# Optimization experiments

Hardware: AMD Instinct MI355X
Metric: run time of the kernel (lower is better)

## Reference

```python
import jax, jax.numpy as jnp
import numpy as np

NUM_EMBEDDINGS = 4096
EMBEDDING_DIM = 256


def setup_inputs() -> dict:
    key = jax.random.key(0)
    k1, k2 = jax.random.split(key)
    inputs = jax.random.normal(k1, (16, 4096, EMBEDDING_DIM), dtype=jnp.float32)
    embeddings = jax.random.normal(k2, (NUM_EMBEDDINGS, EMBEDDING_DIM), dtype=jnp.float32)
    return {"inputs": inputs, "embeddings": embeddings}


def reference(inputs, embeddings):
    input_shape = inputs.shape
    flat = inputs.reshape(-1, EMBEDDING_DIM)                     # [N, D]
    input_sq = jnp.sum(flat * flat, axis=1, keepdims=True)       # [N, 1]
    emb_sq = jnp.sum(embeddings * embeddings, axis=1)            # [K]
    distances = input_sq - 2.0 * (flat @ embeddings.T) + emb_sq  # [N, K]
    encoding_indices = jnp.argmin(distances, axis=1)             # [N]
    quantized = embeddings[encoding_indices].reshape(input_shape)
    encoding_indices = encoding_indices.reshape(input_shape[:-1])
    # use_commitment=False path: codebook loss only (quantized detached)
    loss = jnp.mean((jax.lax.stop_gradient(quantized) - inputs) ** 2)
    # straight-through estimator
    quantized_st = inputs + jax.lax.stop_gradient(quantized - inputs)
    return (quantized_st, loss, encoding_indices)
```

## Files before the change

### kernel.cpp

```cpp
#include <hip/hip_runtime.h>
#include <float.h>
#include <stdint.h>


#define DDIM 256
#define KCODES 4096
#define NROWS 65536
#define QSIZE 16777216
#define NSLOT 64
#define NLBLK 16384
#define GAP_THRESH 0.02f

#define O_FCOUNT 4097
#define O_FLAGS 4100
#define O_IDXF 69636
#define O_LPART 135172
#define O_EMBH 151556
#define O_EMBL 675844
#define O_AH 1200384
#define O_AL 9588992
#define O_KEYS 17977600
#define WS_NEED_FLOATS 18108672ull

typedef short bf16x8 __attribute__((ext_vector_type(8)));
typedef float f32x4 __attribute__((ext_vector_type(4)));

__device__ __forceinline__ void gload_lds16(const void* g, void* l) {
    __builtin_amdgcn_global_load_lds(
        (const __attribute__((address_space(1))) void*)g,
        (__attribute__((address_space(3))) void*)l, 16, 0, 0);
}

__global__ __launch_bounds__(64) void esq_conv(const float* __restrict__ emb,
                                               float* __restrict__ ws,
                                               short* __restrict__ eh,
                                               short* __restrict__ el) {
    int c = blockIdx.x, l = threadIdx.x;
    const float4* e4 = (const float4*)(emb + (size_t)c * DDIM);
    float4 v = e4[l];
    float s = v.x * v.x + v.y * v.y + v.z * v.z + v.w * v.w;
    float f[4] = {v.x, v.y, v.z, v.w};
    uint32_t hu[4], lu[4];
#pragma unroll
    for (int k = 0; k < 4; ++k) {
        uint32_t u = __float_as_uint(f[k]);
        uint32_t h = u & 0xFFFF0000u;
        hu[k] = h;
        lu[k] = __float_as_uint(f[k] - __uint_as_float(h));
    }
    uint2 hv, lv;
    hv.x = __builtin_amdgcn_perm(hu[1], hu[0], 0x07060302u);
    hv.y = __builtin_amdgcn_perm(hu[3], hu[2], 0x07060302u);
    lv.x = __builtin_amdgcn_perm(lu[1], lu[0], 0x07060302u);
    lv.y = __builtin_amdgcn_perm(lu[3], lu[2], 0x07060302u);
    *(uint2*)&eh[(size_t)c * DDIM + l * 4] = hv;
    *(uint2*)&el[(size_t)c * DDIM + l * 4] = lv;
#pragma unroll
    for (int off = 32; off >= 1; off >>= 1) s += __shfl_down(s, off);
    if (l == 0) ws[c] = s;
    if (c == 0 && l == 0) ((int*)ws)[O_FCOUNT] = 0;
}

__device__ __forceinline__ void conv8(float4 a, float4 b,
                                      short* __restrict__ dh,
                                      short* __restrict__ dl) {
    float f[8] = {a.x, a.y, a.z, a.w, b.x, b.y, b.z, b.w};
    uint32_t hu[8], lu[8];
#pragma unroll
    for (int k = 0; k < 8; ++k) {
        uint32_t u = __float_as_uint(f[k]);
        uint32_t h = u & 0xFFFF0000u;
        hu[k] = h;
        lu[k] = __float_as_uint(f[k] - __uint_as_float(h));
    }
    uint4 hv, lv;
    hv.x = __builtin_amdgcn_perm(hu[1], hu[0], 0x07060302u);
    hv.y = __builtin_amdgcn_perm(hu[3], hu[2], 0x07060302u);
    hv.z = __builtin_amdgcn_perm(hu[5], hu[4], 0x07060302u);
    hv.w = __builtin_amdgcn_perm(hu[7], hu[6], 0x07060302u);
    lv.x = __builtin_amdgcn_perm(lu[1], lu[0], 0x07060302u);
    lv.y = __builtin_amdgcn_perm(lu[3], lu[2], 0x07060302u);
    lv.z = __builtin_amdgcn_perm(lu[5], lu[4], 0x07060302u);
    lv.w = __builtin_amdgcn_perm(lu[7], lu[6], 0x07060302u);
    *(uint4*)dh = hv;
    *(uint4*)dl = lv;
}

__device__ __forceinline__ void stage8(const float* __restrict__ p,
                                       short* __restrict__ dh,
                                       short* __restrict__ dl) {
    float4 a = *(const float4*)p;
    float4 b = *(const float4*)(p + 4);
    conv8(a, b, dh, dl);
}

__global__ __launch_bounds__(256) void inp_conv(const float* __restrict__ inp,
                                                short* __restrict__ ahg,
                                                short* __restrict__ alg) {
    size_t g = (size_t)blockIdx.x * 256 + threadIdx.x;
    const float* p = inp + g * 8;
    float4 a = *(const float4*)p;
    float4 b = *(const float4*)(p + 4);
    conv8(a, b, ahg + g * 8, alg + g * 8);
}

__global__ __launch_bounds__(512, 6) void vq_gemm(const short* __restrict__ ahg,
                                                  const short* __restrict__ alg,
                                                  const short* __restrict__ ehg,
                                                  const short* __restrict__ elg,
                                                  const float* __restrict__ esq,
                                                  float2* __restrict__ pmin2,
                                                  int* __restrict__ pidx) {
    __shared__ __align__(16) short Ah[128 * 32];
    __shared__ __align__(16) short Al[128 * 32];
    __shared__ __align__(16) short Bh[128 * 32];
    __shared__ __align__(16) short Bl[128 * 32];

    const int t = threadIdx.x;
    const int mi = blockIdx.x >> 5, ni = blockIdx.x & 31;
    const size_t row0 = (size_t)mi * 128;
    const int col0 = ni * 128;
    const int lane = t & 63, wave = t >> 6;
    const int wm = wave >> 1, wn = wave & 1;
    const int n15 = lane & 15, quad = lane >> 4;
    const int swz = (n15 >> 1) & 3;

    const int r0 = t >> 2, c0 = t & 3;
    const int p0 = c0 ^ ((r0 >> 1) & 3);
    const short* asrch = ahg + (size_t)(row0 + r0) * DDIM + p0 * 8;
    const short* asrcl = alg + (size_t)(row0 + r0) * DDIM + p0 * 8;
    const short* bsrch = ehg + (size_t)(col0 + r0) * DDIM + p0 * 8;
    const short* bsrcl = elg + (size_t)(col0 + r0) * DDIM + p0 * 8;
    const int d0 = t * 8;

    f32x4 acc[2][4];
#pragma unroll
    for (int i = 0; i < 2; ++i)
#pragma unroll
        for (int j = 0; j < 4; ++j) {
            acc[i][j][0] = 0.f; acc[i][j][1] = 0.f;
            acc[i][j][2] = 0.f; acc[i][j][3] = 0.f;
        }

#pragma unroll
    for (int ch = 0; ch < 8; ++ch) {
        __syncthreads();
        gload_lds16(asrch + ch * 32, &Ah[d0]);
        gload_lds16(asrcl + ch * 32, &Al[d0]);
        gload_lds16(bsrch + ch * 32, &Bh[d0]);
        gload_lds16(bsrcl + ch * 32, &Bl[d0]);
        __syncthreads();

        bf16x8 ah[2], al[2];
#pragma unroll
        for (int i = 0; i < 2; ++i) {
            int off = (wm * 32 + i * 16 + n15) * 32 + ((quad ^ swz) * 8);
            ah[i] = *(const bf16x8*)&Ah[off];
            al[i] = *(const bf16x8*)&Al[off];
        }
#pragma unroll
        for (int j = 0; j < 4; ++j) {
            int boff = (wn * 64 + j * 16 + n15) * 32 + ((quad ^ swz) * 8);
            bf16x8 bh = *(const bf16x8*)&Bh[boff];
            bf16x8 bl = *(const bf16x8*)&Bl[boff];
#pragma unroll
            for (int i = 0; i < 2; ++i) {
                acc[i][j] = __builtin_amdgcn_mfma_f32_16x16x32_bf16(ah[i], bh, acc[i][j], 0, 0, 0);
                acc[i][j] = __builtin_amdgcn_mfma_f32_16x16x32_bf16(ah[i], bl, acc[i][j], 0, 0, 0);
                acc[i][j] = __builtin_amdgcn_mfma_f32_16x16x32_bf16(al[i], bh, acc[i][j], 0, 0, 0);
            }
        }
    }

    float esqv[4];
#pragma unroll
    for (int j = 0; j < 4; ++j) esqv[j] = esq[col0 + wn * 64 + j * 16 + n15];

#pragma unroll
    for (int i = 0; i < 2; ++i) {
#pragma unroll
        for (int reg = 0; reg < 4; ++reg) {
            float m1 = FLT_MAX, m2 = FLT_MAX;
            int bi = 0;
#pragma unroll
            for (int j = 0; j < 4; ++j) {
                float d = esqv[j] - 2.0f * acc[i][j][reg];
                int code = col0 + wn * 64 + j * 16 + n15;
                if (d < m1) { m2 = m1; m1 = d; bi = code; }
                else if (d < m2) { m2 = d; }
            }
#pragma unroll
            for (int off = 1; off < 16; off <<= 1) {
                float om1 = __shfl_xor(m1, off);
                float om2 = __shfl_xor(m2, off);
                int obi = __shfl_xor(bi, off);
                bool take = (om1 < m1) || (om1 == m1 && obi < bi);
                if (take) { m2 = fminf(m1, om2); m1 = om1; bi = obi; }
                else      { m2 = fminf(om1, m2); }
            }
            if (n15 == 0) {
                int rg = (int)row0 + wm * 32 + i * 16 + quad * 4 + reg;
                int slot = ni * 2 + wn;
                pmin2[(size_t)slot * NROWS + rg] = make_float2(m1, m2);
                pidx[(size_t)slot * NROWS + rg] = bi;
            }
        }
    }
}

__global__ __launch_bounds__(256, 2) void vq_gemm_fb(const float* __restrict__ inp,
                                                     const short* __restrict__ ehg,
                                                     const short* __restrict__ elg,
                                                     const float* __restrict__ esq,
                                                     float2* __restrict__ pmin2,
                                                     int* __restrict__ pidx) {
    __shared__ __align__(16) short Ah[128 * 32];
    __shared__ __align__(16) short Al[128 * 32];
    __shared__ __align__(16) short Bh[128 * 32];
    __shared__ __align__(16) short Bl[128 * 32];

    const int t = threadIdx.x;
    const int mi = blockIdx.x >> 5, ni = blockIdx.x & 31;
    const size_t row0 = (size_t)mi * 128;
    const int col0 = ni * 128;
    const int lane = t & 63, wave = t >> 6;
    const int wm = wave >> 1, wn = wave & 1;
    const int n15 = lane & 15, quad = lane >> 4;
    const int swz = (n15 >> 1) & 3;

    const int ar0 = t >> 2, ac0 = t & 3;
    const int ap0 = ac0 ^ ((ar0 >> 1) & 3);
    const int ar1 = (t + 256) >> 2, ac1 = ac0;
    const int ap1 = ac1 ^ ((ar1 >> 1) & 3);
    const float* asrc0 = inp + (row0 + ar0) * DDIM + ac0 * 8;
    const float* asrc1 = inp + (row0 + ar1) * DDIM + ac1 * 8;
    short* adst0h = &Ah[ar0 * 32 + ap0 * 8];
    short* adst0l = &Al[ar0 * 32 + ap0 * 8];
    short* adst1h = &Ah[ar1 * 32 + ap1 * 8];
    short* adst1l = &Al[ar1 * 32 + ap1 * 8];
    const int br0 = ar0, bp0 = ac0, bk0 = bp0 ^ ((br0 >> 1) & 3);
    const int br1 = ar1, bp1 = ac1, bk1 = bp1 ^ ((br1 >> 1) & 3);
    const short* bsrc0h = ehg + (size_t)(col0 + br0) * DDIM + bk0 * 8;
    const short* bsrc0l = elg + (size_t)(col0 + br0) * DDIM + bk0 * 8;
    const short* bsrc1h = ehg + (size_t)(col0 + br1) * DDIM + bk1 * 8;
    const short* bsrc1l = elg + (size_t)(col0 + br1) * DDIM + bk1 * 8;

    f32x4 acc[4][4];
#pragma unroll
    for (int i = 0; i < 4; ++i)
#pragma unroll
        for (int j = 0; j < 4; ++j) {
            acc[i][j][0] = 0.f; acc[i][j][1] = 0.f;
            acc[i][j][2] = 0.f; acc[i][j][3] = 0.f;
        }

#pragma unroll
    for (int ch = 0; ch < 8; ++ch) {
        __syncthreads();
        gload_lds16(bsrc0h + ch * 32, &Bh[t * 8]);
        gload_lds16(bsrc0l + ch * 32, &Bl[t * 8]);
        gload_lds16(bsrc1h + ch * 32, &Bh[(t + 256) * 8]);
        gload_lds16(bsrc1l + ch * 32, &Bl[(t + 256) * 8]);
        stage8(asrc0 + ch * 32, adst0h, adst0l);
        stage8(asrc1 + ch * 32, adst1h, adst1l);
        __syncthreads();

        bf16x8 ah[4], al[4];
#pragma unroll
        for (int i = 0; i < 4; ++i) {
            int off = (wm * 64 + i * 16 + n15) * 32 + ((quad ^ swz) * 8);
            ah[i] = *(const bf16x8*)&Ah[off];
            al[i] = *(const bf16x8*)&Al[off];
        }
#pragma unroll
        for (int j = 0; j < 4; ++j) {
            int boff = (wn * 64 + j * 16 + n15) * 32 + ((quad ^ swz) * 8);
            bf16x8 bh = *(const bf16x8*)&Bh[boff];
            bf16x8 bl = *(const bf16x8*)&Bl[boff];
#pragma unroll
            for (int i = 0; i < 4; ++i) {
                acc[i][j] = __builtin_amdgcn_mfma_f32_16x16x32_bf16(ah[i], bh, acc[i][j], 0, 0, 0);
                acc[i][j] = __builtin_amdgcn_mfma_f32_16x16x32_bf16(ah[i], bl, acc[i][j], 0, 0, 0);
                acc[i][j] = __builtin_amdgcn_mfma_f32_16x16x32_bf16(al[i], bh, acc[i][j], 0, 0, 0);
            }
        }
    }

    float esqv[4];
#pragma unroll
    for (int j = 0; j < 4; ++j) esqv[j] = esq[col0 + wn * 64 + j * 16 + n15];

#pragma unroll
    for (int i = 0; i < 4; ++i) {
#pragma unroll
        for (int reg = 0; reg < 4; ++reg) {
            float m1 = FLT_MAX, m2 = FLT_MAX;
            int bi = 0;
#pragma unroll
            for (int j = 0; j < 4; ++j) {
                float d = esqv[j] - 2.0f * acc[i][j][reg];
                int code = col0 + wn * 64 + j * 16 + n15;
                if (d < m1) { m2 = m1; m1 = d; bi = code; }
                else if (d < m2) { m2 = d; }
            }
#pragma unroll
            for (int off = 1; off < 16; off <<= 1) {
                float om1 = __shfl_xor(m1, off);
                float om2 = __shfl_xor(m2, off);
                int obi = __shfl_xor(bi, off);
                bool take = (om1 < m1) || (om1 == m1 && obi < bi);
                if (take) { m2 = fminf(m1, om2); m1 = om1; bi = obi; }
                else      { m2 = fminf(om1, m2); }
            }
            if (n15 == 0) {
                int rg = (int)row0 + wm * 64 + i * 16 + quad * 4 + reg;
                int slot = ni * 2 + wn;
                pmin2[(size_t)slot * NROWS + rg] = make_float2(m1, m2);
                pidx[(size_t)slot * NROWS + rg] = bi;
            }
        }
    }
}

__global__ __launch_bounds__(256) void vq_reduce(const float2* __restrict__ pmin2,
                                                 const int* __restrict__ pidx,
                                                 int* __restrict__ idx_final,
                                                 int* __restrict__ flags,
                                                 int* __restrict__ fcount,
                                                 unsigned long long* __restrict__ keys) {
    int row = blockIdx.x * 256 + threadIdx.x;
    float m1 = FLT_MAX, m2 = FLT_MAX;
    int bi = 0;
    for (int nb = 0; nb < NSLOT; ++nb) {
        float2 p = pmin2[(size_t)nb * NROWS + row];
        int pi = pidx[(size_t)nb * NROWS + row];
        if (p.x < m1) { m2 = fminf(m1, p.y); m1 = p.x; bi = pi; }
        else          { m2 = fminf(m2, p.x); }
    }
    idx_final[row] = bi;
    if (m2 - m1 < GAP_THRESH) {
        int s = atomicAdd(fcount, 1);
        flags[s] = row;
        if (keys) keys[s] = 0xFFFFFFFFFFFFFFFFull;
    }
}

__global__ __launch_bounds__(256) void vq_recheck2(const float* __restrict__ inp,
                                                   const float* __restrict__ emb,
                                                   const float* __restrict__ esq,
                                                   const int* __restrict__ flags,
                                                   const int* __restrict__ fcount,
                                                   unsigned long long* __restrict__ keys) {
    __shared__ float4 xs[4][64];
    __shared__ unsigned long long wbest[4][4];
    const int t = threadIdx.x;
    const int cnt = *fcount;
    const int ngrp = (cnt + 3) >> 2;
    const int total = ngrp * 16;
    for (int wi = blockIdx.x; wi < total; wi += gridDim.x) {
        const int gi = wi >> 4, cb = wi & 15;
        const int base = gi * 4;
        const int nr = (cnt - base < 4) ? (cnt - base) : 4;
        __syncthreads();
        {
            int rr = t >> 6, l = t & 63;
            if (rr < nr)
                xs[rr][l] = ((const float4*)inp)[(size_t)flags[base + rr] * 64 + l];
        }
        __syncthreads();
        const int c = cb * 256 + t;
        const float4* e4 = (const float4*)emb + (size_t)c * 64;
        float dot0 = 0.f, dot1 = 0.f, dot2 = 0.f, dot3 = 0.f;
        for (int d4 = 0; d4 < 64; ++d4) {
            float4 e = e4[d4];
            float4 x0 = xs[0][d4];
            float4 x1 = xs[1][d4];
            float4 x2 = xs[2][d4];
            float4 x3 = xs[3][d4];
            dot0 += e.x * x0.x; dot0 += e.y * x0.y; dot0 += e.z * x0.z; dot0 += e.w * x0.w;
            dot1 += e.x * x1.x; dot1 += e.y * x1.y; dot1 += e.z * x1.z; dot1 += e.w * x1.w;
            dot2 += e.x * x2.x; dot2 += e.y * x2.y; dot2 += e.z * x2.z; dot2 += e.w * x2.w;
            dot3 += e.x * x3.x; dot3 += e.y * x3.y; dot3 += e.z * x3.z; dot3 += e.w * x3.w;
        }
        float dts[4] = {dot0, dot1, dot2, dot3};
        const float ec = esq[c];
#pragma unroll
        for (int rr = 0; rr < 4; ++rr) {
            float d = ec - 2.0f * dts[rr];
            unsigned u = __float_as_uint(d);
            unsigned skey = (u & 0x80000000u) ? ~u : (u | 0x80000000u);
            unsigned long long k = ((unsigned long long)skey << 32) | (unsigned)c;
#pragma unroll
            for (int off = 1; off < 64; off <<= 1) {
                unsigned long long o = __shfl_xor(k, off);
                if (o < k) k = o;
            }
            if ((t & 63) == 0) wbest[t >> 6][rr] = k;
        }
        __syncthreads();
        if (t < nr) {
            unsigned long long b = wbest[0][t];
            if (wbest[1][t] < b) b = wbest[1][t];
            if (wbest[2][t] < b) b = wbest[2][t];
            if (wbest[3][t] < b) b = wbest[3][t];
            atomicMin(&keys[base + t], b);
        }
    }
}

__global__ __launch_bounds__(256) void vq_unpack(const int* __restrict__ flags,
                                                 const int* __restrict__ fcount,
                                                 const unsigned long long* __restrict__ keys,
                                                 int* __restrict__ idx_final) {
    int i = blockIdx.x * 256 + threadIdx.x;
    if (i < *fcount) idx_final[flags[i]] = (int)(keys[i] & 0xFFFFFFFFull);
}

__global__ __launch_bounds__(256) void vq_recheck(const float* __restrict__ inp,
                                                  const float* __restrict__ emb,
                                                  const float* __restrict__ esq,
                                                  const int* __restrict__ flags,
                                                  const int* __restrict__ fcount,
                                                  int* __restrict__ idx_final) {
    __shared__ float4 xs[64];
    __shared__ float sv[4];
    __shared__ int si[4];
    const int t = threadIdx.x;
    const int cnt = *fcount;
    for (int f = blockIdx.x; f < cnt; f += gridDim.x) {
        int row = flags[f];
        __syncthreads();
        if (t < 64) xs[t] = ((const float4*)inp)[(size_t)row * 64 + t];
        __syncthreads();
        float m1 = FLT_MAX;
        int bi = 0x7FFFFFFF;
        for (int cc = 0; cc < 16; ++cc) {
            int c = cc * 256 + t;
            const float4* e4 = (const float4*)emb + (size_t)c * 64;
            float dot = 0.f;
            for (int d4 = 0; d4 < 64; ++d4) {
                float4 e = e4[d4];
                float4 x = xs[d4];
                dot += e.x * x.x; dot += e.y * x.y;
                dot += e.z * x.z; dot += e.w * x.w;
            }
            float d = esq[c] - 2.0f * dot;
            if (d < m1 || (d == m1 && c < bi)) { m1 = d; bi = c; }
        }
#pragma unroll
        for (int off = 1; off < 64; off <<= 1) {
            float om = __shfl_xor(m1, off);
            int ob = __shfl_xor(bi, off);
            if (om < m1 || (om == m1 && ob < bi)) { m1 = om; bi = ob; }
        }
        if ((t & 63) == 0) { sv[t >> 6] = m1; si[t >> 6] = bi; }
        __syncthreads();
        if (t == 0) {
            for (int w = 1; w < 4; ++w)
                if (sv[w] < m1 || (sv[w] == m1 && si[w] < bi)) { m1 = sv[w]; bi = si[w]; }
            idx_final[row] = bi;
        }
    }
}

__global__ __launch_bounds__(256) void vq_gather(const float* __restrict__ inp,
                                                 const float* __restrict__ emb,
                                                 const int* __restrict__ idx_final,
                                                 float* __restrict__ out,
                                                 float* __restrict__ loss_part) {
    __shared__ float wsum[4];
    size_t gid = (size_t)blockIdx.x * 256 + threadIdx.x;
    int row = (int)(gid >> 6), c4 = (int)(gid & 63);
    int k = idx_final[row];
    float4 e = ((const float4*)emb)[(size_t)k * 64 + c4];
    float4 x = ((const float4*)inp)[gid];
    ((float4*)out)[gid] = e;
    float dx = e.x - x.x, dy = e.y - x.y, dz = e.z - x.z, dw = e.w - x.w;
    float ls = dx * dx + dy * dy + dz * dz + dw * dw;
#pragma unroll
    for (int off = 32; off >= 1; off >>= 1) ls += __shfl_down(ls, off);
    if ((threadIdx.x & 63) == 0) wsum[threadIdx.x >> 6] = ls;
    if (c4 == 0) out[(size_t)QSIZE + 1 + row] = (float)k;
    __syncthreads();
    if (threadIdx.x == 0)
        loss_part[blockIdx.x] = wsum[0] + wsum[1] + wsum[2] + wsum[3];
}

__global__ __launch_bounds__(256) void loss_kernel(const float* __restrict__ loss_part,
                                                   float* __restrict__ out) {
    __shared__ float sw[4];
    int t = threadIdx.x;
    float s = 0.0f;
    for (int i = t; i < NLBLK; i += 256) s += loss_part[i];
#pragma unroll
    for (int off = 32; off >= 1; off >>= 1) s += __shfl_down(s, off);
    if ((t & 63) == 0) sw[t >> 6] = s;
    __syncthreads();
    if (t == 0)
        out[QSIZE] = (sw[0] + sw[1] + sw[2] + sw[3]) * (1.0f / 16777216.0f);
}

extern "C" void kernel_launch(void* const* d_in, const int* in_sizes, int n_in,
                              void* d_out, int out_size, void* d_ws, size_t ws_size,
                              hipStream_t stream) {
    const float* inp = (const float*)d_in[0];
    const float* emb = (const float*)d_in[1];
    float* out = (float*)d_out;
    float* ws = (float*)d_ws;

    float* esq = ws;
    int* fcount = (int*)ws + O_FCOUNT;
    int* flags = (int*)ws + O_FLAGS;
    int* idx_final = (int*)ws + O_IDXF;
    float* loss_part = ws + O_LPART;
    short* eh = (short*)(ws + O_EMBH);
    short* el = (short*)(ws + O_EMBL);

    float2* pmin2 = (float2*)out;
    int* pidx = (int*)out + 8388608;

    hipLaunchKernelGGL(esq_conv, dim3(KCODES), dim3(64), 0, stream, emb, ws, eh, el);

    if (ws_size >= WS_NEED_FLOATS * 4ull) {
        short* ah = (short*)(ws + O_AH);
        short* al = (short*)(ws + O_AL);
        unsigned long long* keys = (unsigned long long*)(ws + O_KEYS);
        hipLaunchKernelGGL(inp_conv, dim3(8192), dim3(256), 0, stream, inp, ah, al);
        hipLaunchKernelGGL(vq_gemm, dim3((NROWS / 128) * 32), dim3(512), 0, stream,
                           ah, al, eh, el, esq, pmin2, pidx);
        hipLaunchKernelGGL(vq_reduce, dim3(NROWS / 256), dim3(256), 0, stream,
                           pmin2, pidx, idx_final, flags, fcount, keys);
        hipLaunchKernelGGL(vq_recheck2, dim3(8192), dim3(256), 0, stream,
                           inp, emb, esq, flags, fcount, keys);
        hipLaunchKernelGGL(vq_unpack, dim3(NROWS / 256), dim3(256), 0, stream,
                           flags, fcount, keys, idx_final);
    } else {
        hipLaunchKernelGGL(vq_gemm_fb, dim3((NROWS / 128) * 32), dim3(256), 0, stream,
                           inp, eh, el, esq, pmin2, pidx);
        hipLaunchKernelGGL(vq_reduce, dim3(NROWS / 256), dim3(256), 0, stream,
                           pmin2, pidx, idx_final, flags, fcount,
                           (unsigned long long*)nullptr);
        hipLaunchKernelGGL(vq_recheck, dim3(256), dim3(256), 0, stream,
                           inp, emb, esq, flags, fcount, idx_final);
    }

    hipLaunchKernelGGL(vq_gather, dim3(NLBLK), dim3(256), 0, stream,
                       inp, emb, idx_final, out, loss_part);
    hipLaunchKernelGGL(loss_kernel, dim3(1), dim3(256), 0, stream, loss_part, out);
}
```

Before: 673.5 us.

## Merge wn halves in GEMM epilogue and fuse input/codebook conversion kernels

The GEMM epilogue now combines the two column-half warps' top-2 minima through shared memory before writing, which halves the partial slots (64 to 32) written to global memory and read by the reduce kernel. The separate embedding and input conversion kernels are merged into one launch, with extra blocks handling codebook rows. The fallback path keeps 64 slots via a dedicated reduce kernel. This adds two block barriers and LDS traffic in the epilogue in exchange for less global partial traffic and one fewer launch.

```diff
diff --git a/kernel.cpp b/kernel.cpp
--- a/kernel.cpp
+++ b/kernel.cpp
@@ -7,7 +7,8 @@
 #define KCODES 4096
 #define NROWS 65536
 #define QSIZE 16777216
-#define NSLOT 64
+#define NSLOT 32
+#define NSLOT_FB 64
 #define NLBLK 16384
 #define GAP_THRESH 0.02f
 
@@ -29,36 +30,6 @@
     __builtin_amdgcn_global_load_lds(
         (const __attribute__((address_space(1))) void*)g,
         (__attribute__((address_space(3))) void*)l, 16, 0, 0);
-}
-
-__global__ __launch_bounds__(64) void esq_conv(const float* __restrict__ emb,
-                                               float* __restrict__ ws,
-                                               short* __restrict__ eh,
-                                               short* __restrict__ el) {
-    int c = blockIdx.x, l = threadIdx.x;
-    const float4* e4 = (const float4*)(emb + (size_t)c * DDIM);
-    float4 v = e4[l];
-    float s = v.x * v.x + v.y * v.y + v.z * v.z + v.w * v.w;
-    float f[4] = {v.x, v.y, v.z, v.w};
-    uint32_t hu[4], lu[4];
-#pragma unroll
-    for (int k = 0; k < 4; ++k) {
-        uint32_t u = __float_as_uint(f[k]);
-        uint32_t h = u & 0xFFFF0000u;
-        hu[k] = h;
-        lu[k] = __float_as_uint(f[k] - __uint_as_float(h));
-    }
-    uint2 hv, lv;
-    hv.x = __builtin_amdgcn_perm(hu[1], hu[0], 0x07060302u);
-    hv.y = __builtin_amdgcn_perm(hu[3], hu[2], 0x07060302u);
-    lv.x = __builtin_amdgcn_perm(lu[1], lu[0], 0x07060302u);
-    lv.y = __builtin_amdgcn_perm(lu[3], lu[2], 0x07060302u);
-    *(uint2*)&eh[(size_t)c * DDIM + l * 4] = hv;
-    *(uint2*)&el[(size_t)c * DDIM + l * 4] = lv;
-#pragma unroll
-    for (int off = 32; off >= 1; off >>= 1) s += __shfl_down(s, off);
-    if (l == 0) ws[c] = s;
-    if (c == 0 && l == 0) ((int*)ws)[O_FCOUNT] = 0;
 }
 
 __device__ __forceinline__ void conv8(float4 a, float4 b,
@@ -94,14 +65,77 @@
     conv8(a, b, dh, dl);
 }
 
-__global__ __launch_bounds__(256) void inp_conv(const float* __restrict__ inp,
-                                                short* __restrict__ ahg,
-                                                short* __restrict__ alg) {
-    size_t g = (size_t)blockIdx.x * 256 + threadIdx.x;
-    const float* p = inp + g * 8;
-    float4 a = *(const float4*)p;
-    float4 b = *(const float4*)(p + 4);
-    conv8(a, b, ahg + g * 8, alg + g * 8);
+__global__ __launch_bounds__(64) void esq_conv(const float* __restrict__ emb,
+                                               float* __restrict__ ws,
+                                               short* __restrict__ eh,
+                                               short* __restrict__ el) {
+    int c = blockIdx.x, l = threadIdx.x;
+    const float4* e4 = (const float4*)(emb + (size_t)c * DDIM);
+    float4 v = e4[l];
+    float s = v.x * v.x + v.y * v.y + v.z * v.z + v.w * v.w;
+    float f[4] = {v.x, v.y, v.z, v.w};
+    uint32_t hu[4], lu[4];
+#pragma unroll
+    for (int k = 0; k < 4; ++k) {
+        uint32_t u = __float_as_uint(f[k]);
+        uint32_t h = u & 0xFFFF0000u;
+        hu[k] = h;
+        lu[k] = __float_as_uint(f[k] - __uint_as_float(h));
+    }
+    uint2 hv, lv;
+    hv.x = __builtin_amdgcn_perm(hu[1], hu[0], 0x07060302u);
+    hv.y = __builtin_amdgcn_perm(hu[3], hu[2], 0x07060302u);
+    lv.x = __builtin_amdgcn_perm(lu[1], lu[0], 0x07060302u);
+    lv.y = __builtin_amdgcn_perm(lu[3], lu[2], 0x07060302u);
+    *(uint2*)&eh[(size_t)c * DDIM + l * 4] = hv;
+    *(uint2*)&el[(size_t)c * DDIM + l * 4] = lv;
+#pragma unroll
+    for (int off = 32; off >= 1; off >>= 1) s += __shfl_down(s, off);
+    if (l == 0) ws[c] = s;
+    if (c == 0 && l == 0) ((int*)ws)[O_FCOUNT] = 0;
+}
+
+__global__ __launch_bounds__(256) void prep_conv(const float* __restrict__ inp,
+                                                 const float* __restrict__ emb,
+                                                 float* __restrict__ ws,
+                                                 short* __restrict__ eh,
+                                                 short* __restrict__ el,
+                                                 short* __restrict__ ahg,
+                                                 short* __restrict__ alg) {
+    int b = blockIdx.x, t = threadIdx.x;
+    if (b < 8192) {
+        size_t g = (size_t)b * 256 + t;
+        const float* p = inp + g * 8;
+        float4 a = *(const float4*)p;
+        float4 bb = *(const float4*)(p + 4);
+        conv8(a, bb, ahg + g * 8, alg + g * 8);
+        return;
+    }
+    int c = (b - 8192) * 4 + (t >> 6);
+    int l = t & 63;
+    const float4* e4 = (const float4*)(emb + (size_t)c * DDIM);
+    float4 v = e4[l];
+    float s = v.x * v.x + v.y * v.y + v.z * v.z + v.w * v.w;
+    float f[4] = {v.x, v.y, v.z, v.w};
+    uint32_t hu[4], lu[4];
+#pragma unroll
+    for (int k = 0; k < 4; ++k) {
+        uint32_t u = __float_as_uint(f[k]);
+        uint32_t h = u & 0xFFFF0000u;
+        hu[k] = h;
+        lu[k] = __float_as_uint(f[k] - __uint_as_float(h));
+    }
+    uint2 hv, lv;
+    hv.x = __builtin_amdgcn_perm(hu[1], hu[0], 0x07060302u);
+    hv.y = __builtin_amdgcn_perm(hu[3], hu[2], 0x07060302u);
+    lv.x = __builtin_amdgcn_perm(lu[1], lu[0], 0x07060302u);
+    lv.y = __builtin_amdgcn_perm(lu[3], lu[2], 0x07060302u);
+    *(uint2*)&eh[(size_t)c * DDIM + l * 4] = hv;
+    *(uint2*)&el[(size_t)c * DDIM + l * 4] = lv;
+#pragma unroll
+    for (int off = 32; off >= 1; off >>= 1) s += __shfl_down(s, off);
+    if (l == 0) ws[c] = s;
+    if (c == 0 && l == 0) ((int*)ws)[O_FCOUNT] = 0;
 }
 
 __global__ __launch_bounds__(512, 6) void vq_gemm(const short* __restrict__ ahg,
@@ -176,6 +210,8 @@
 #pragma unroll
     for (int j = 0; j < 4; ++j) esqv[j] = esq[col0 + wn * 64 + j * 16 + n15];
 
+    float fm1[8], fm2[8];
+    int fbi[8];
 #pragma unroll
     for (int i = 0; i < 2; ++i) {
 #pragma unroll
@@ -198,12 +234,39 @@
                 if (take) { m2 = fminf(m1, om2); m1 = om1; bi = obi; }
                 else      { m2 = fminf(om1, m2); }
             }
-            if (n15 == 0) {
-                int rg = (int)row0 + wm * 32 + i * 16 + quad * 4 + reg;
-                int slot = ni * 2 + wn;
-                pmin2[(size_t)slot * NROWS + rg] = make_float2(m1, m2);
-                pidx[(size_t)slot * NROWS + rg] = bi;
-            }
+            fm1[i * 4 + reg] = m1;
+            fm2[i * 4 + reg] = m2;
+            fbi[i * 4 + reg] = bi;
+        }
+    }
+
+    float* s1 = (float*)Ah;
+    float* s2 = (float*)Al;
+    int* sb = (int*)Bh;
+    __syncthreads();
+    if (wn == 1 && n15 == 0) {
+#pragma unroll
+        for (int k = 0; k < 8; ++k) {
+            int local = (k >> 2) * 16 + quad * 4 + (k & 3);
+            int s = wm * 32 + local;
+            s1[s] = fm1[k]; s2[s] = fm2[k]; sb[s] = fbi[k];
+        }
+    }
+    __syncthreads();
+    if (wn == 0 && n15 == 0) {
+#pragma unroll
+        for (int k = 0; k < 8; ++k) {
+            int local = (k >> 2) * 16 + quad * 4 + (k & 3);
+            int s = wm * 32 + local;
+            float m1 = fm1[k], m2 = fm2[k];
+            int bi = fbi[k];
+            float p1 = s1[s], p2 = s2[s];
+            int pb = sb[s];
+            if (p1 < m1) { m2 = fminf(m1, p2); m1 = p1; bi = pb; }
+            else         { m2 = fminf(m2, p1); }
+            int rg = (int)row0 + wm * 32 + local;
+            pmin2[(size_t)ni * NROWS + rg] = make_float2(m1, m2);
+            pidx[(size_t)ni * NROWS + rg] = bi;
         }
     }
 }
@@ -341,7 +404,28 @@
     if (m2 - m1 < GAP_THRESH) {
         int s = atomicAdd(fcount, 1);
         flags[s] = row;
-        if (keys) keys[s] = 0xFFFFFFFFFFFFFFFFull;
+        keys[s] = 0xFFFFFFFFFFFFFFFFull;
+    }
+}
+
+__global__ __launch_bounds__(256) void vq_reduce_fb(const float2* __restrict__ pmin2,
+                                                    const int* __restrict__ pidx,
+                                                    int* __restrict__ idx_final,
+                                                    int* __restrict__ flags,
+                                                    int* __restrict__ fcount) {
+    int row = blockIdx.x * 256 + threadIdx.x;
+    float m1 = FLT_MAX, m2 = FLT_MAX;
+    int bi = 0;
+    for (int nb = 0; nb < NSLOT_FB; ++nb) {
+        float2 p = pmin2[(size_t)nb * NROWS + row];
+        int pi = pidx[(size_t)nb * NROWS + row];
+        if (p.x < m1) { m2 = fminf(m1, p.y); m1 = p.x; bi = pi; }
+        else          { m2 = fminf(m2, p.x); }
+    }
+    idx_final[row] = bi;
+    if (m2 - m1 < GAP_THRESH) {
+        int s = atomicAdd(fcount, 1);
+        flags[s] = row;
     }
 }
 
@@ -516,16 +600,14 @@
     short* eh = (short*)(ws + O_EMBH);
     short* el = (short*)(ws + O_EMBL);
 
-    float2* pmin2 = (float2*)out;
-    int* pidx = (int*)out + 8388608;
-
-    hipLaunchKernelGGL(esq_conv, dim3(KCODES), dim3(64), 0, stream, emb, ws, eh, el);
-
     if (ws_size >= WS_NEED_FLOATS * 4ull) {
         short* ah = (short*)(ws + O_AH);
         short* al = (short*)(ws + O_AL);
         unsigned long long* keys = (unsigned long long*)(ws + O_KEYS);
-        hipLaunchKernelGGL(inp_conv, dim3(8192), dim3(256), 0, stream, inp, ah, al);
+        float2* pmin2 = (float2*)out;
+        int* pidx = (int*)out + 4194304;
+        hipLaunchKernelGGL(prep_conv, dim3(8192 + KCODES / 4), dim3(256), 0, stream,
+                           inp, emb, ws, eh, el, ah, al);
         hipLaunchKernelGGL(vq_gemm, dim3((NROWS / 128) * 32), dim3(512), 0, stream,
                            ah, al, eh, el, esq, pmin2, pidx);
         hipLaunchKernelGGL(vq_reduce, dim3(NROWS / 256), dim3(256), 0, stream,
@@ -535,11 +617,13 @@
         hipLaunchKernelGGL(vq_unpack, dim3(NROWS / 256), dim3(256), 0, stream,
                            flags, fcount, keys, idx_final);
     } else {
+        float2* pmin2 = (float2*)out;
+        int* pidx = (int*)out + 8388608;
+        hipLaunchKernelGGL(esq_conv, dim3(KCODES), dim3(64), 0, stream, emb, ws, eh, el);
         hipLaunchKernelGGL(vq_gemm_fb, dim3((NROWS / 128) * 32), dim3(256), 0, stream,
                            inp, eh, el, esq, pmin2, pidx);
-        hipLaunchKernelGGL(vq_reduce, dim3(NROWS / 256), dim3(256), 0, stream,
-                           pmin2, pidx, idx_final, flags, fcount,
-                           (unsigned long long*)nullptr);
+        hipLaunchKernelGGL(vq_reduce_fb, dim3(NROWS / 256), dim3(256), 0, stream,
+                           pmin2, pidx, idx_final, flags, fcount);
         hipLaunchKernelGGL(vq_recheck, dim3(256), dim3(256), 0, stream,
                            inp, emb, esq, flags, fcount, idx_final);
     }
```

Result: no change. 664.0 us (-1.4%).
